# Optimization experiments

Measured on AMD Instinct MI355X. Metric: run time of the kernel, lower is better.

The kernel has to match this reference:

```python
import jax, jax.numpy as jnp
import numpy as np

N, T, DYN, STAT, H = 50000, 24, 16, 8, 64
E = 1_600_000


def gru_last(x, Wih, Whh, bih, bhh):
    # x: [N, T, DYN]; torch GRU gate order: r, z, n
    gx = jnp.einsum('ntd,gd->ntg', x, Wih) + bih  # [N, T, 3H]
    h0 = jnp.zeros((x.shape[0], H), x.dtype)

    def step(h, gx_t):
        gh = h @ Whh.T + bhh  # [N, 3H]
        xr, xz, xn = jnp.split(gx_t, 3, axis=-1)
        hr, hz, hn = jnp.split(gh, 3, axis=-1)
        r = jax.nn.sigmoid(xr + hr)
        z = jax.nn.sigmoid(xz + hz)
        n = jnp.tanh(xn + r * hn)
        h_new = (1.0 - z) * n + z * h
        return h_new, None

    h_last, _ = jax.lax.scan(step, h0, jnp.swapaxes(gx, 0, 1))  # scan over T
    return h_last  # [N, H]


def gcn_layer(x, W, b, src, dst, w):
    h = x @ W  # [N, out]
    msg = h[src] * w[:, None]  # gather + weight  [E, out]
    agg = jax.ops.segment_sum(msg, dst, num_segments=N)  # scatter-add
    return agg + b


def setup_inputs() -> dict:
    key = jax.random.key(0)
    ks = jax.random.split(key, 16)
    s = 0.1
    return {
        'x_dyn': jax.random.normal(ks[0], (N, T, DYN), jnp.float32),
        'x_stat': jax.random.normal(ks[1], (N, STAT), jnp.float32),
        'edge_index': jax.random.randint(ks[2], (2, E), 0, N, jnp.int32),
        'edge_weight': jax.random.uniform(ks[3], (E,), jnp.float32),
        'Wih': jax.random.normal(ks[4], (3 * H, DYN), jnp.float32) * s,
        'Whh': jax.random.normal(ks[5], (3 * H, H), jnp.float32) * s,
        'bih': jnp.zeros((3 * H,), jnp.float32),
        'bhh': jnp.zeros((3 * H,), jnp.float32),
        'W1': jax.random.normal(ks[6], (H + STAT, H), jnp.float32) * s,
        'b1': jnp.zeros((H,), jnp.float32),
        'W2': jax.random.normal(ks[7], (H, H), jnp.float32) * s,
        'b2': jnp.zeros((H,), jnp.float32),
        'Wa': jax.random.normal(ks[8], (H, 1), jnp.float32) * s,
        'ba': jnp.zeros((1,), jnp.float32),
        'Wp': jax.random.normal(ks[9], (H, 1), jnp.float32) * s,
        'bp': jnp.zeros((1,), jnp.float32),
    }


def reference(x_dyn, x_stat, edge_index, edge_weight,
              Wih, Whh, bih, bhh, W1, b1, W2, b2, Wa, ba, Wp, bp):
    src, dst = edge_index[0], edge_index[1]
    z = gru_last(x_dyn, Wih, Whh, bih, bhh)            # [N, H]
    h = jnp.concatenate([z, x_stat], axis=1)           # [N, H+STAT]
    h = jax.nn.relu(gcn_layer(h, W1, b1, src, dst, edge_weight))
    h = jax.nn.relu(gcn_layer(h, W2, b2, src, dst, edge_weight))
    # dropout omitted (eval mode)
    aqi = (h @ Wa + ba)[:, 0]
    pm = (h @ Wp + bp)[:, 0]
    return aqi, pm
```

## Files before the change

kernel.cpp:

```cpp
#include <hip/hip_runtime.h>
#include <cstdint>
#include <cstddef>

#define NNODES 50000
#define TT 24
#define DYNF 16
#define STATF 8
#define HDIM 64
#define NEDGES 1600000
#define NB 32
#define GRU_BLOCKS ((NNODES + NB - 1) / NB)
#define FILL_CHUNK 1024
#define FILL_CHUNKS ((NEDGES + FILL_CHUNK - 1) / FILL_CHUNK)
#define CAP 80

typedef __attribute__((ext_vector_type(8))) short bf16x8;
typedef __attribute__((ext_vector_type(4))) float f32x4;
typedef __attribute__((ext_vector_type(2))) float f32x2;
typedef __attribute__((ext_vector_type(2))) unsigned u32x2;

__device__ __forceinline__ unsigned short f2bf(float f) {
    unsigned u = __float_as_uint(f);
    u = (u + 0x7FFFu + ((u >> 16) & 1u)) >> 16;
    return (unsigned short)u;
}
__device__ __forceinline__ float bf2f(unsigned short s) {
    return __uint_as_float((unsigned)s << 16);
}
__device__ __forceinline__ bf16x8 cvt8(const float* __restrict__ p) {
    bf16x8 r;
    #pragma unroll
    for (int i = 0; i < 8; ++i) r[i] = (short)f2bf(p[i]);
    return r;
}
__device__ __forceinline__ bf16x8 zero8() {
    bf16x8 z;
    #pragma unroll
    for (int i = 0; i < 8; ++i) z[i] = 0;
    return z;
}
__device__ __forceinline__ float fast_tanh(float x) {
    float e = __expf(2.f * x);
    return 1.f - 2.f * __builtin_amdgcn_rcpf(e + 1.f);
}

__global__ __launch_bounds__(256, 4) void gru_fill_kernel(
    const float* __restrict__ x_dyn, const float* __restrict__ x_stat,
    const float* __restrict__ Wih, const float* __restrict__ Whh,
    const float* __restrict__ bih, const float* __restrict__ bhh,
    const float* __restrict__ W1, unsigned short* __restrict__ t1,
    const int* __restrict__ srcv, const int* __restrict__ dstv,
    const float* __restrict__ ew, int* __restrict__ cursor,
    unsigned* __restrict__ csr)
{
    constexpr int S_H = 72;
    constexpr int S_X = 40;
    __shared__ short hbuf[2][NB * S_H];
    __shared__ short xbuf[2][NB * S_X];

    const int tid = (int)threadIdx.x;

    if ((int)blockIdx.x >= GRU_BLOCKS) {
        const int fb = (int)blockIdx.x - GRU_BLOCKS;
        const int range = fb & 7;
        const int chunk = fb >> 3;
        const int base = chunk * FILL_CHUNK;
        const int lo = range * (NNODES / 8);
        const int hi = (range == 7) ? NNODES : lo + (NNODES / 8);
        #pragma unroll
        for (int j = 0; j < FILL_CHUNK / 256; ++j) {
            const int e = base + j * 256 + tid;
            if (e < NEDGES) {
                const int d = dstv[e];
                if (d >= lo && d < hi) {
                    const int s = __builtin_nontemporal_load(srcv + e);
                    const float we = __builtin_nontemporal_load(ew + e);
                    const int pos = atomicAdd(&cursor[d], 1);
                    if (pos < CAP)
                        csr[(size_t)d * CAP + pos] =
                            (unsigned)s | ((unsigned)f2bf(we) << 16);
                }
            }
        }
        return;
    }

    const int lane = tid & 63;
    const int w = __builtin_amdgcn_readfirstlane(tid >> 6);
    const int col = lane & 15;
    const int quad = lane >> 4;
    const int node0 = (int)blockIdx.x * NB;

    bf16x8 Bh[3][2];
    bf16x8 Bx[3];
    #pragma unroll
    for (int g = 0; g < 3; ++g) {
        const int n = (w + g * 4) * 16 + col;
        #pragma unroll
        for (int kt = 0; kt < 2; ++kt)
            Bh[g][kt] = cvt8(Whh + (size_t)n * HDIM + kt * 32 + quad * 8);
        Bx[g] = (quad < 2) ? cvt8(Wih + (size_t)n * DYNF + quad * 8) : zero8();
    }

    const int jg = w * 16 + col;
    const float b_r  = bih[jg]        + bhh[jg];
    const float b_z  = bih[HDIM + jg] + bhh[HDIM + jg];
    const float b_xn = bih[2 * HDIM + jg];
    const float b_hn = bhh[2 * HDIM + jg];

    for (int i = tid; i < NB * S_H; i += 256) hbuf[0][i] = 0;

    auto stage_x = [&](int t, int b) {
        const int nd = tid >> 3, c = tid & 7;
        int node = node0 + nd;
        if (node >= NNODES) node = 0;
        const f32x2 v = __builtin_nontemporal_load(
            reinterpret_cast<const f32x2*>(
                x_dyn + (size_t)node * (TT * DYNF) + t * DYNF + c * 2));
        unsigned pk = (unsigned)f2bf(v[0]) | ((unsigned)f2bf(v[1]) << 16);
        *reinterpret_cast<unsigned*>(&xbuf[b][nd * S_X + c * 2]) = pk;
        *reinterpret_cast<unsigned*>(&xbuf[b][nd * S_X + 16 + c * 2]) = 0u;
    };
    stage_x(0, 0);

    float hprev[2][4];
    #pragma unroll
    for (int mt = 0; mt < 2; ++mt)
        #pragma unroll
        for (int r = 0; r < 4; ++r) hprev[mt][r] = 0.f;

    for (int t = 0; t < TT; ++t) {
        const int rb = t & 1;
        __syncthreads();

        f32x4 accr[2], accz[2], accnh[2], accnx[2];
        #pragma unroll
        for (int mt = 0; mt < 2; ++mt) {
            const int nd = mt * 16 + col;
            const bf16x8 a0 = *reinterpret_cast<const bf16x8*>(&hbuf[rb][nd * S_H + quad * 8]);
            const bf16x8 a1 = *reinterpret_cast<const bf16x8*>(&hbuf[rb][nd * S_H + 32 + quad * 8]);
            const bf16x8 ax = *reinterpret_cast<const bf16x8*>(&xbuf[rb][nd * S_X + quad * 8]);
            const f32x4 z4 = {0.f, 0.f, 0.f, 0.f};
            accr[mt]  = __builtin_amdgcn_mfma_f32_16x16x32_bf16(a0, Bh[0][0], z4, 0, 0, 0);
            accr[mt]  = __builtin_amdgcn_mfma_f32_16x16x32_bf16(a1, Bh[0][1], accr[mt], 0, 0, 0);
            accr[mt]  = __builtin_amdgcn_mfma_f32_16x16x32_bf16(ax, Bx[0],    accr[mt], 0, 0, 0);
            accz[mt]  = __builtin_amdgcn_mfma_f32_16x16x32_bf16(a0, Bh[1][0], z4, 0, 0, 0);
            accz[mt]  = __builtin_amdgcn_mfma_f32_16x16x32_bf16(a1, Bh[1][1], accz[mt], 0, 0, 0);
            accz[mt]  = __builtin_amdgcn_mfma_f32_16x16x32_bf16(ax, Bx[1],    accz[mt], 0, 0, 0);
            accnh[mt] = __builtin_amdgcn_mfma_f32_16x16x32_bf16(a0, Bh[2][0], z4, 0, 0, 0);
            accnh[mt] = __builtin_amdgcn_mfma_f32_16x16x32_bf16(a1, Bh[2][1], accnh[mt], 0, 0, 0);
            accnx[mt] = __builtin_amdgcn_mfma_f32_16x16x32_bf16(ax, Bx[2],    z4, 0, 0, 0);
        }

        if (t + 1 < TT) stage_x(t + 1, rb ^ 1);

        #pragma unroll
        for (int mt = 0; mt < 2; ++mt) {
            #pragma unroll
            for (int r = 0; r < 4; ++r) {
                const float dr = 1.f + __expf(-(accr[mt][r] + b_r));
                const float dz = 1.f + __expf(-(accz[mt][r] + b_z));
                const float q  = __builtin_amdgcn_rcpf(dr * dz);
                const float R  = q * dz;
                const float Z  = q * dr;
                const float Nn = fast_tanh(accnx[mt][r] + b_xn + R * (accnh[mt][r] + b_hn));
                const float hn = Nn + Z * (hprev[mt][r] - Nn);
                hprev[mt][r] = hn;
                hbuf[rb ^ 1][(mt * 16 + quad * 4 + r) * S_H + jg] = (short)f2bf(hn);
            }
        }
    }
    __syncthreads();

    bf16x8 Bw0, Bw1, Bw2;
    #pragma unroll
    for (int j = 0; j < 8; ++j) {
        Bw0[j] = (short)f2bf(W1[(size_t)(quad * 8 + j) * HDIM + jg]);
        Bw1[j] = (short)f2bf(W1[(size_t)(32 + quad * 8 + j) * HDIM + jg]);
    }
    if (quad == 0) {
        #pragma unroll
        for (int j = 0; j < 8; ++j)
            Bw2[j] = (short)f2bf(W1[(size_t)(HDIM + j) * HDIM + jg]);
    } else {
        Bw2 = zero8();
    }

    #pragma unroll
    for (int mt = 0; mt < 2; ++mt) {
        const int nd = mt * 16 + col;
        const bf16x8 a0 = *reinterpret_cast<const bf16x8*>(&hbuf[0][nd * S_H + quad * 8]);
        const bf16x8 a1 = *reinterpret_cast<const bf16x8*>(&hbuf[0][nd * S_H + 32 + quad * 8]);
        bf16x8 axs;
        if (quad == 0) {
            int node = node0 + nd;
            if (node >= NNODES) node = 0;
            axs = cvt8(x_stat + (size_t)node * STATF);
        } else {
            axs = zero8();
        }
        const f32x4 z4 = {0.f, 0.f, 0.f, 0.f};
        f32x4 aw;
        aw = __builtin_amdgcn_mfma_f32_16x16x32_bf16(a0, Bw0, z4, 0, 0, 0);
        aw = __builtin_amdgcn_mfma_f32_16x16x32_bf16(a1, Bw1, aw, 0, 0, 0);
        aw = __builtin_amdgcn_mfma_f32_16x16x32_bf16(axs, Bw2, aw, 0, 0, 0);
        #pragma unroll
        for (int r = 0; r < 4; ++r) {
            const int node = node0 + mt * 16 + quad * 4 + r;
            if (node < NNODES) t1[(size_t)node * HDIM + jg] = f2bf(aw[r]);
        }
    }
}

__global__ __launch_bounds__(256) void gather_transform_kernel(
    const unsigned short* __restrict__ tsrc, const int* __restrict__ cursor,
    const unsigned* __restrict__ csr, const float* __restrict__ b1,
    const float* __restrict__ W2, unsigned short* __restrict__ out)
{
    __shared__ float aggL[16][68];
    const int tid  = (int)threadIdx.x;
    const int lane = tid & 63;
    const int w    = tid >> 6;
    const int q    = lane >> 4;
    const int f    = lane & 15;
    const int col  = lane & 15;
    const int quad = lane >> 4;
    const int node0 = (int)blockIdx.x * 16;
    const int jg = w * 16 + col;

    bf16x8 Bw0, Bw1;
    float bk0[8], bk1[8];
    #pragma unroll
    for (int j = 0; j < 8; ++j) {
        Bw0[j] = (short)f2bf(W2[(size_t)(quad * 8 + j) * HDIM + jg]);
        Bw1[j] = (short)f2bf(W2[(size_t)(32 + quad * 8 + j) * HDIM + jg]);
        bk0[j] = b1[quad * 8 + j];
        bk1[j] = b1[32 + quad * 8 + j];
    }

    for (int i = 0; i < 4; ++i) {
        const int nloc = w * 4 + i;
        const int node = node0 + nloc;
        const int beg = node * CAP;
        const int cnt = min(cursor[node], CAP);
        const int end = beg + cnt;
        float a0 = 0.f, a1 = 0.f, a2 = 0.f, a3 = 0.f;
        int p = beg;
        for (; p + 8 <= end; p += 8) {
            const unsigned e0 = csr[p + q];
            const unsigned e1 = csr[p + 4 + q];
            const u32x2 r0 = *reinterpret_cast<const u32x2*>(
                tsrc + (size_t)(e0 & 0xFFFFu) * HDIM + 4 * f);
            const u32x2 r1 = *reinterpret_cast<const u32x2*>(
                tsrc + (size_t)(e1 & 0xFFFFu) * HDIM + 4 * f);
            const float w0 = __uint_as_float(e0 & 0xFFFF0000u);
            const float w1 = __uint_as_float(e1 & 0xFFFF0000u);
            a0 += w0 * bf2f((unsigned short)(r0[0] & 0xFFFFu));
            a1 += w0 * bf2f((unsigned short)(r0[0] >> 16));
            a2 += w0 * bf2f((unsigned short)(r0[1] & 0xFFFFu));
            a3 += w0 * bf2f((unsigned short)(r0[1] >> 16));
            a0 += w1 * bf2f((unsigned short)(r1[0] & 0xFFFFu));
            a1 += w1 * bf2f((unsigned short)(r1[0] >> 16));
            a2 += w1 * bf2f((unsigned short)(r1[1] & 0xFFFFu));
            a3 += w1 * bf2f((unsigned short)(r1[1] >> 16));
        }
        if (p + 4 <= end) {
            const unsigned e0 = csr[p + q];
            const u32x2 r0 = *reinterpret_cast<const u32x2*>(
                tsrc + (size_t)(e0 & 0xFFFFu) * HDIM + 4 * f);
            const float w0 = __uint_as_float(e0 & 0xFFFF0000u);
            a0 += w0 * bf2f((unsigned short)(r0[0] & 0xFFFFu));
            a1 += w0 * bf2f((unsigned short)(r0[0] >> 16));
            a2 += w0 * bf2f((unsigned short)(r0[1] & 0xFFFFu));
            a3 += w0 * bf2f((unsigned short)(r0[1] >> 16));
            p += 4;
        }
        const int rem = end - p;
        if (q < rem) {
            const unsigned e0 = csr[p + q];
            const u32x2 r0 = *reinterpret_cast<const u32x2*>(
                tsrc + (size_t)(e0 & 0xFFFFu) * HDIM + 4 * f);
            const float w0 = __uint_as_float(e0 & 0xFFFF0000u);
            a0 += w0 * bf2f((unsigned short)(r0[0] & 0xFFFFu));
            a1 += w0 * bf2f((unsigned short)(r0[0] >> 16));
            a2 += w0 * bf2f((unsigned short)(r0[1] & 0xFFFFu));
            a3 += w0 * bf2f((unsigned short)(r0[1] >> 16));
        }
        a0 += __shfl_xor(a0, 16, 64); a0 += __shfl_xor(a0, 32, 64);
        a1 += __shfl_xor(a1, 16, 64); a1 += __shfl_xor(a1, 32, 64);
        a2 += __shfl_xor(a2, 16, 64); a2 += __shfl_xor(a2, 32, 64);
        a3 += __shfl_xor(a3, 16, 64); a3 += __shfl_xor(a3, 32, 64);
        if (lane < 16) {
            f32x4 o; o[0] = a0; o[1] = a1; o[2] = a2; o[3] = a3;
            *reinterpret_cast<f32x4*>(&aggL[nloc][4 * f]) = o;
        }
    }
    __syncthreads();

    bf16x8 fa0, fa1;
    #pragma unroll
    for (int j = 0; j < 8; ++j) {
        fa0[j] = (short)f2bf(fmaxf(aggL[col][quad * 8 + j] + bk0[j], 0.f));
        fa1[j] = (short)f2bf(fmaxf(aggL[col][32 + quad * 8 + j] + bk1[j], 0.f));
    }
    const f32x4 z4 = {0.f, 0.f, 0.f, 0.f};
    f32x4 aw;
    aw = __builtin_amdgcn_mfma_f32_16x16x32_bf16(fa0, Bw0, z4, 0, 0, 0);
    aw = __builtin_amdgcn_mfma_f32_16x16x32_bf16(fa1, Bw1, aw, 0, 0, 0);
    #pragma unroll
    for (int r = 0; r < 4; ++r)
        out[(size_t)(node0 + quad * 4 + r) * HDIM + jg] = f2bf(aw[r]);
}

__global__ __launch_bounds__(256) void gather_head_kernel(
    const unsigned short* __restrict__ tsrc, const int* __restrict__ cursor,
    const unsigned* __restrict__ csr,
    const float* __restrict__ b2, const float* __restrict__ Wa,
    const float* __restrict__ ba, const float* __restrict__ Wp,
    const float* __restrict__ bp, float* __restrict__ out)
{
    const int node = blockIdx.x * 4 + (threadIdx.x >> 6);
    const int lane = (int)threadIdx.x & 63;
    const int q = lane >> 4;
    const int f = lane & 15;
    if (node >= NNODES) return;
    const int beg = node * CAP;
    const int cnt = min(cursor[node], CAP);
    const int end = beg + cnt;
    float a0 = 0.f, a1 = 0.f, a2 = 0.f, a3 = 0.f;
    int p = beg;
    for (; p + 8 <= end; p += 8) {
        const unsigned e0 = csr[p + q];
        const unsigned e1 = csr[p + 4 + q];
        const u32x2 r0 = *reinterpret_cast<const u32x2*>(
            tsrc + (size_t)(e0 & 0xFFFFu) * HDIM + 4 * f);
        const u32x2 r1 = *reinterpret_cast<const u32x2*>(
            tsrc + (size_t)(e1 & 0xFFFFu) * HDIM + 4 * f);
        const float w0 = __uint_as_float(e0 & 0xFFFF0000u);
        const float w1 = __uint_as_float(e1 & 0xFFFF0000u);
        a0 += w0 * bf2f((unsigned short)(r0[0] & 0xFFFFu));
        a1 += w0 * bf2f((unsigned short)(r0[0] >> 16));
        a2 += w0 * bf2f((unsigned short)(r0[1] & 0xFFFFu));
        a3 += w0 * bf2f((unsigned short)(r0[1] >> 16));
        a0 += w1 * bf2f((unsigned short)(r1[0] & 0xFFFFu));
        a1 += w1 * bf2f((unsigned short)(r1[0] >> 16));
        a2 += w1 * bf2f((unsigned short)(r1[1] & 0xFFFFu));
        a3 += w1 * bf2f((unsigned short)(r1[1] >> 16));
    }
    if (p + 4 <= end) {
        const unsigned e0 = csr[p + q];
        const u32x2 r0 = *reinterpret_cast<const u32x2*>(
            tsrc + (size_t)(e0 & 0xFFFFu) * HDIM + 4 * f);
        const float w0 = __uint_as_float(e0 & 0xFFFF0000u);
        a0 += w0 * bf2f((unsigned short)(r0[0] & 0xFFFFu));
        a1 += w0 * bf2f((unsigned short)(r0[0] >> 16));
        a2 += w0 * bf2f((unsigned short)(r0[1] & 0xFFFFu));
        a3 += w0 * bf2f((unsigned short)(r0[1] >> 16));
        p += 4;
    }
    const int rem = end - p;
    if (q < rem) {
        const unsigned e0 = csr[p + q];
        const u32x2 r0 = *reinterpret_cast<const u32x2*>(
            tsrc + (size_t)(e0 & 0xFFFFu) * HDIM + 4 * f);
        const float w0 = __uint_as_float(e0 & 0xFFFF0000u);
        a0 += w0 * bf2f((unsigned short)(r0[0] & 0xFFFFu));
        a1 += w0 * bf2f((unsigned short)(r0[0] >> 16));
        a2 += w0 * bf2f((unsigned short)(r0[1] & 0xFFFFu));
        a3 += w0 * bf2f((unsigned short)(r0[1] >> 16));
    }
    a0 += __shfl_xor(a0, 16, 64); a0 += __shfl_xor(a0, 32, 64);
    a1 += __shfl_xor(a1, 16, 64); a1 += __shfl_xor(a1, 32, 64);
    a2 += __shfl_xor(a2, 16, 64); a2 += __shfl_xor(a2, 32, 64);
    a3 += __shfl_xor(a3, 16, 64); a3 += __shfl_xor(a3, 32, 64);

    const f32x4 bb = *reinterpret_cast<const f32x4*>(b2 + 4 * f);
    const f32x4 wa = *reinterpret_cast<const f32x4*>(Wa + 4 * f);
    const f32x4 wp = *reinterpret_cast<const f32x4*>(Wp + 4 * f);
    const float h0 = fmaxf(a0 + bb[0], 0.f);
    const float h1 = fmaxf(a1 + bb[1], 0.f);
    const float h2 = fmaxf(a2 + bb[2], 0.f);
    const float h3 = fmaxf(a3 + bb[3], 0.f);
    float sa = h0 * wa[0] + h1 * wa[1] + h2 * wa[2] + h3 * wa[3];
    float sp = h0 * wp[0] + h1 * wp[1] + h2 * wp[2] + h3 * wp[3];
    #pragma unroll
    for (int off = 1; off < 16; off <<= 1) {
        sa += __shfl_xor(sa, off, 64);
        sp += __shfl_xor(sp, off, 64);
    }
    if (lane == 0) {
        out[node] = sa + ba[0];
        out[NNODES + node] = sp + bp[0];
    }
}

extern "C" void kernel_launch(void* const* d_in, const int* in_sizes, int n_in,
                              void* d_out, int out_size, void* d_ws, size_t ws_size,
                              hipStream_t stream)
{
    const float* x_dyn  = (const float*)d_in[0];
    const float* x_stat = (const float*)d_in[1];
    const int*   eidx   = (const int*)  d_in[2];
    const float* ew     = (const float*)d_in[3];
    const float* Wih    = (const float*)d_in[4];
    const float* Whh    = (const float*)d_in[5];
    const float* bih    = (const float*)d_in[6];
    const float* bhh    = (const float*)d_in[7];
    const float* W1     = (const float*)d_in[8];
    const float* b1     = (const float*)d_in[9];
    const float* W2     = (const float*)d_in[10];
    const float* b2     = (const float*)d_in[11];
    const float* Wa     = (const float*)d_in[12];
    const float* ba     = (const float*)d_in[13];
    const float* Wp     = (const float*)d_in[14];
    const float* bp     = (const float*)d_in[15];

    const int* srcv = eidx;
    const int* dstv = eidx + NEDGES;

    const size_t NH = (size_t)NNODES * HDIM;
    float* ws   = (float*)d_ws;
    unsigned short* t1 = (unsigned short*)ws;
    unsigned short* t2 = (unsigned short*)(ws + NH / 2);
    unsigned* csr = (unsigned*)(ws + NH);
    int* cursor = (int*)(csr + (size_t)NNODES * CAP);

    dim3 blk(256);

    hipMemsetAsync(cursor, 0, (size_t)NNODES * sizeof(int), stream);

    gru_fill_kernel<<<dim3(GRU_BLOCKS + FILL_CHUNKS * 8), blk, 0, stream>>>(
        x_dyn, x_stat, Wih, Whh, bih, bhh, W1, t1,
        srcv, dstv, ew, cursor, csr);

    gather_transform_kernel<<<dim3(NNODES / 16), blk, 0, stream>>>(
        t1, cursor, csr, b1, W2, t2);

    gather_head_kernel<<<dim3((NNODES + 3) / 4), blk, 0, stream>>>(
        t2, cursor, csr, b2, Wa, ba, Wp, bp, (float*)d_out);
}
```

Before: 378.9 us.

## Replace 8-way dst-range CSR fill with two-pass binning via LDS staging

New measurement: 376.9 us. About the same (-0.5%).

```diff
diff --git a/kernel.cpp b/kernel.cpp
--- a/kernel.cpp
+++ b/kernel.cpp
@@ -13,6 +13,9 @@
 #define FILL_CHUNK 1024
 #define FILL_CHUNKS ((NEDGES + FILL_CHUNK - 1) / FILL_CHUNK)
 #define CAP 80
+#define SLICE (NNODES / 8)
+#define BINCAP 210000
+#define STAGE 192
 
 typedef __attribute__((ext_vector_type(8))) short bf16x8;
 typedef __attribute__((ext_vector_type(4))) float f32x4;
@@ -50,37 +53,57 @@
     const float* __restrict__ bih, const float* __restrict__ bhh,
     const float* __restrict__ W1, unsigned short* __restrict__ t1,
     const int* __restrict__ srcv, const int* __restrict__ dstv,
-    const float* __restrict__ ew, int* __restrict__ cursor,
-    unsigned* __restrict__ csr)
+    const float* __restrict__ ew, int* __restrict__ binCnt,
+    u32x2* __restrict__ bins)
 {
     constexpr int S_H = 72;
     constexpr int S_X = 40;
     __shared__ short hbuf[2][NB * S_H];
     __shared__ short xbuf[2][NB * S_X];
+    __shared__ u32x2 stg[8][STAGE];
+    __shared__ int lcnt[8];
+    __shared__ int gbase[8];
 
     const int tid = (int)threadIdx.x;
 
     if ((int)blockIdx.x >= GRU_BLOCKS) {
         const int fb = (int)blockIdx.x - GRU_BLOCKS;
-        const int range = fb & 7;
-        const int chunk = fb >> 3;
-        const int base = chunk * FILL_CHUNK;
-        const int lo = range * (NNODES / 8);
-        const int hi = (range == 7) ? NNODES : lo + (NNODES / 8);
+        const int base = fb * FILL_CHUNK;
+        if (tid < 8) lcnt[tid] = 0;
+        __syncthreads();
         #pragma unroll
         for (int j = 0; j < FILL_CHUNK / 256; ++j) {
             const int e = base + j * 256 + tid;
             if (e < NEDGES) {
-                const int d = dstv[e];
-                if (d >= lo && d < hi) {
-                    const int s = __builtin_nontemporal_load(srcv + e);
-                    const float we = __builtin_nontemporal_load(ew + e);
-                    const int pos = atomicAdd(&cursor[d], 1);
-                    if (pos < CAP)
-                        csr[(size_t)d * CAP + pos] =
-                            (unsigned)s | ((unsigned)f2bf(we) << 16);
+                const int d = __builtin_nontemporal_load(dstv + e);
+                const int s = __builtin_nontemporal_load(srcv + e);
+                const float we = __builtin_nontemporal_load(ew + e);
+                const int b = d / SLICE;
+                u32x2 rec;
+                rec[0] = (unsigned)s | ((unsigned)f2bf(we) << 16);
+                rec[1] = (unsigned)(d - b * SLICE);
+                const int pos = atomicAdd(&lcnt[b], 1);
+                if (pos < STAGE) {
+                    stg[b][pos] = rec;
+                } else {
+                    const int gp = atomicAdd(&binCnt[b], 1);
+                    if (gp < BINCAP) bins[(size_t)b * BINCAP + gp] = rec;
                 }
             }
+        }
+        __syncthreads();
+        if (tid < 8) {
+            const int n = min(lcnt[tid], STAGE);
+            gbase[tid] = atomicAdd(&binCnt[tid], n);
+        }
+        __syncthreads();
+        #pragma unroll 1
+        for (int b = 0; b < 8; ++b) {
+            const int n = min(lcnt[b], STAGE);
+            const int gb = gbase[b];
+            for (int i = tid; i < n; i += 256)
+                if (gb + i < BINCAP)
+                    bins[(size_t)b * BINCAP + gb + i] = stg[b][i];
         }
         return;
     }
@@ -209,6 +232,23 @@
             const int node = node0 + mt * 16 + quad * 4 + r;
             if (node < NNODES) t1[(size_t)node * HDIM + jg] = f2bf(aw[r]);
         }
+    }
+}
+
+__global__ __launch_bounds__(256) void fill_scatter_kernel(
+    const u32x2* __restrict__ bins, const int* __restrict__ binCnt,
+    int* __restrict__ cursor, unsigned* __restrict__ csr)
+{
+    const int slice = (int)blockIdx.x & 7;
+    const int sub   = (int)blockIdx.x >> 3;
+    const int lo    = slice * SLICE;
+    const int cnt   = min(binCnt[slice], BINCAP);
+    const u32x2* __restrict__ mybin = bins + (size_t)slice * BINCAP;
+    for (int i = sub * 256 + (int)threadIdx.x; i < cnt; i += 96 * 256) {
+        const u32x2 r = __builtin_nontemporal_load(mybin + i);
+        const int d = lo + (int)r[1];
+        const int pos = atomicAdd(&cursor[d], 1);
+        if (pos < CAP) csr[(size_t)d * CAP + pos] = r[0];
     }
 }
 
@@ -418,20 +458,23 @@
     const int* srcv = eidx;
     const int* dstv = eidx + NEDGES;
 
-    const size_t NH = (size_t)NNODES * HDIM;
-    float* ws   = (float*)d_ws;
-    unsigned short* t1 = (unsigned short*)ws;
-    unsigned short* t2 = (unsigned short*)(ws + NH / 2);
-    unsigned* csr = (unsigned*)(ws + NH);
+    unsigned short* t1 = (unsigned short*)d_ws;
+    unsigned short* t2 = t1 + (size_t)NNODES * HDIM;
+    unsigned* csr = (unsigned*)(t2 + (size_t)NNODES * HDIM);
     int* cursor = (int*)(csr + (size_t)NNODES * CAP);
+    int* binCnt = cursor + NNODES;
+    u32x2* bins = (u32x2*)(binCnt + 16);
 
     dim3 blk(256);
 
-    hipMemsetAsync(cursor, 0, (size_t)NNODES * sizeof(int), stream);
-
-    gru_fill_kernel<<<dim3(GRU_BLOCKS + FILL_CHUNKS * 8), blk, 0, stream>>>(
+    hipMemsetAsync(cursor, 0, (size_t)(NNODES + 16) * sizeof(int), stream);
+
+    gru_fill_kernel<<<dim3(GRU_BLOCKS + FILL_CHUNKS), blk, 0, stream>>>(
         x_dyn, x_stat, Wih, Whh, bih, bhh, W1, t1,
-        srcv, dstv, ew, cursor, csr);
+        srcv, dstv, ew, binCnt, bins);
+
+    fill_scatter_kernel<<<dim3(8 * 96), blk, 0, stream>>>(
+        bins, binCnt, cursor, csr);
 
     gather_transform_kernel<<<dim3(NNODES / 16), blk, 0, stream>>>(
         t1, cursor, csr, b1, W2, t2);
```
